# Optimization experiments

Measured on AMD Instinct MI355X. Metric: run time of the kernel, lower is better.

## Reference

```python
import jax, jax.numpy as jnp
import numpy as np

VOCAB = 128000
H = 256
L = 65536  # complete binary tree: 2**16 leaves -> 16 merge levels


def setup_inputs() -> dict:
    key = jax.random.key(0)
    ks = jax.random.split(key, 10)
    tokens = jax.random.randint(ks[0], (L,), 0, VOCAB)
    emb = jax.random.normal(ks[1], (VOCAB, H), dtype=jnp.float32) * 0.05
    # 5 gate projections per side (r_l, r_r, z_l, z_r, z), torch Linear layout (out, in)
    WL = jax.random.normal(ks[2], (5, H, H), dtype=jnp.float32) * 0.05
    WR = jax.random.normal(ks[3], (5, H, H), dtype=jnp.float32) * 0.05
    bL = jax.random.normal(ks[4], (5, H), dtype=jnp.float32) * 0.05
    bR = jax.random.normal(ks[5], (5, H), dtype=jnp.float32) * 0.05
    # candidate projections self.l / self.r
    Wlh = jax.random.normal(ks[6], (H, H), dtype=jnp.float32) * 0.05
    Wrh = jax.random.normal(ks[7], (H, H), dtype=jnp.float32) * 0.05
    blh = jax.random.normal(ks[8], (H,), dtype=jnp.float32) * 0.05
    brh = jax.random.normal(ks[9], (H,), dtype=jnp.float32) * 0.05
    return {"tokens": tokens, "emb": emb, "WL": WL, "WR": WR, "bL": bL,
            "bR": bR, "Wlh": Wlh, "Wrh": Wrh, "blh": blh, "brh": brh}


def reference(tokens, emb, WL, WR, bL, bR, Wlh, Wrh, blh, brh):
    cur = emb[tokens]  # [L, H] leaf states (embedding lookup)
    n_levels = int(np.log2(cur.shape[0]))
    bias = (bL + bR)[:, None, :]  # [5, 1, H]
    for _ in range(n_levels):
        left = cur[0::2]   # [N, H]
        right = cur[1::2]  # [N, H]
        # all 5 sigmoid gates in one batched contraction (torch Linear: x @ W.T + b)
        pre = (jnp.einsum('nh,goh->gno', left, WL)
               + jnp.einsum('nh,goh->gno', right, WR) + bias)  # [5, N, H]
        g = jax.nn.sigmoid(pre)
        r_l, r_r, z_l, z_r, z = g[0], g[1], g[2], g[3], g[4]
        h_tilde = jnp.tanh((r_l * left) @ Wlh.T + (r_r * right) @ Wrh.T + blh + brh)
        cur = z_l * left + z_r * right + z * h_tilde
    h = cur[0]  # [H] root state
    return (h, h, h)
```

## Files before the change

kernel.cpp:

```cpp
#include <hip/hip_runtime.h>
#include <hip/hip_bf16.h>

#define H 256
#define K2 512
#define BM 32
#define THREADS 512
#define HK2 (H * K2)

typedef __attribute__((ext_vector_type(8))) short short8;
typedef __attribute__((ext_vector_type(4))) float f32x4;

struct __align__(8) S4 { short x, y, z, w; };

__device__ __forceinline__ short f2bf(float f) {
    union { float f; unsigned u; } v; v.f = f;
    unsigned r = v.u + 0x7fffu + ((v.u >> 16) & 1u);
    return (short)(r >> 16);
}
__device__ __forceinline__ float bf2f(short s) {
    union { unsigned u; float f; } v; v.u = ((unsigned)(unsigned short)s) << 16;
    return v.f;
}
__device__ __forceinline__ float sigm(float x) {
    return 1.f / (1.f + __expf(-x));
}
__device__ __forceinline__ float tanh_f(float x) {
    float e = __expf(2.f * x);
    return 1.f - 2.f / (e + 1.f);
}
__device__ __forceinline__ int swz(int row, int kbytes) {
    return ((row << 10) + kbytes) ^ ((row & 7) << 4);
}

__global__ void prep_kernel(const float* __restrict__ WL, const float* __restrict__ WR,
                            const float* __restrict__ Wlh, const float* __restrict__ Wrh,
                            const float* __restrict__ bL, const float* __restrict__ bR,
                            const float* __restrict__ blh, const float* __restrict__ brh,
                            short* __restrict__ W1, short* __restrict__ W2,
                            float* __restrict__ pb, float* __restrict__ hb) {
    int i = blockIdx.x * blockDim.x + threadIdx.x;
    const int nW1 = 5 * HK2;
    if (i < nW1) {
        int g = i / HK2;
        int rem = i % HK2;
        int o = rem / K2, k = rem % K2;
        float v = (k < H) ? WL[(g * H + o) * H + k] : WR[(g * H + o) * H + (k - H)];
        W1[i] = f2bf(v);
        return;
    }
    int j = i - nW1;
    if (j < HK2) {
        int o = j / K2, k = j % K2;
        float v = (k < H) ? Wlh[o * H + k] : Wrh[o * H + (k - H)];
        W2[j] = f2bf(v);
        return;
    }
    int p = j - HK2;
    if (p < 5 * H) { pb[p] = bL[p] + bR[p]; return; }
    int q = p - 5 * H;
    if (q < H) { hb[q] = blh[q] + brh[q]; }
}

__global__ __launch_bounds__(THREADS, 2) void level_kernel(
    const float* __restrict__ curIn, const int* __restrict__ tokens,
    const float* __restrict__ emb, float* __restrict__ curOut,
    const short* __restrict__ W1, const short* __restrict__ W2,
    const float* __restrict__ pb, const float* __restrict__ hb, int N) {
    __shared__ __align__(16) short A1[BM * K2];
    __shared__ __align__(16) short A2[BM * K2];
    const int tid = threadIdx.x;
    const int n0 = blockIdx.x * BM;

#pragma unroll
    for (int it = 0; it < 8; ++it) {
        int c = tid + it * THREADS;
        int r = c >> 6;
        int col = (c & 63) << 2;
        int gr = 2 * n0 + r;
        float4 v = make_float4(0.f, 0.f, 0.f, 0.f);
        if (gr < 2 * N) {
            const float* src = tokens ? (emb + (size_t)tokens[gr] * H)
                                      : (curIn + (size_t)gr * H);
            v = *(const float4*)(src + col);
        }
        int row = r >> 1;
        int kel = ((r & 1) << 8) | col;
        S4 s; s.x = f2bf(v.x); s.y = f2bf(v.y); s.z = f2bf(v.z); s.w = f2bf(v.w);
        *(S4*)((char*)A1 + swz(row, kel * 2)) = s;
    }
    __syncthreads();

    const int wave = tid >> 6, lane = tid & 63;
    const int l15 = lane & 15, khalf = lane >> 4;
    const int col0 = wave * 32;

    f32x4 acc1[2][2][2];
#pragma unroll
    for (int g = 0; g < 2; ++g)
#pragma unroll
        for (int rt = 0; rt < 2; ++rt)
#pragma unroll
            for (int ct = 0; ct < 2; ++ct)
                acc1[g][rt][ct] = (f32x4){0.f, 0.f, 0.f, 0.f};

    const short* b1p[2][2];
#pragma unroll
    for (int g = 0; g < 2; ++g)
#pragma unroll
        for (int ct = 0; ct < 2; ++ct)
            b1p[g][ct] = W1 + g * HK2 + (size_t)(col0 + ct * 16 + l15) * K2 + khalf * 8;

#pragma unroll
    for (int kk = 0; kk < 16; ++kk) {
        short8 a[2];
#pragma unroll
        for (int rt = 0; rt < 2; ++rt)
            a[rt] = *(const short8*)((const char*)A1 + swz(rt * 16 + l15, kk * 64 + khalf * 16));
        short8 b[2][2];
#pragma unroll
        for (int g = 0; g < 2; ++g)
#pragma unroll
            for (int ct = 0; ct < 2; ++ct)
                b[g][ct] = *(const short8*)(b1p[g][ct] + kk * 32);
#pragma unroll
        for (int g = 0; g < 2; ++g)
#pragma unroll
            for (int rt = 0; rt < 2; ++rt)
#pragma unroll
                for (int ct = 0; ct < 2; ++ct)
                    acc1[g][rt][ct] = __builtin_amdgcn_mfma_f32_16x16x32_bf16(
                        a[rt], b[g][ct], acc1[g][rt][ct], 0, 0, 0);
    }

#pragma unroll
    for (int g = 0; g < 2; ++g)
#pragma unroll
        for (int ct = 0; ct < 2; ++ct) {
            int col = col0 + ct * 16 + l15;
            float bias = pb[g * H + col];
            int koff2 = ((g << 8) | col) * 2;
#pragma unroll
            for (int rt = 0; rt < 2; ++rt)
#pragma unroll
                for (int j = 0; j < 4; ++j) {
                    int row = rt * 16 + khalf * 4 + j;
                    float rg = sigm(acc1[g][rt][ct][j] + bias);
                    float xv = bf2f(*(const short*)((const char*)A1 + swz(row, koff2)));
                    *(short*)((char*)A2 + swz(row, koff2)) = f2bf(rg * xv);
                }
        }
    __syncthreads();

    f32x4 acc2[2][2];
#pragma unroll
    for (int rt = 0; rt < 2; ++rt)
#pragma unroll
        for (int ct = 0; ct < 2; ++ct)
            acc2[rt][ct] = (f32x4){0.f, 0.f, 0.f, 0.f};

    const short* b2p[2];
#pragma unroll
    for (int ct = 0; ct < 2; ++ct)
        b2p[ct] = W2 + (size_t)(col0 + ct * 16 + l15) * K2 + khalf * 8;

#pragma unroll
    for (int kk = 0; kk < 16; ++kk) {
        short8 a[2];
#pragma unroll
        for (int rt = 0; rt < 2; ++rt)
            a[rt] = *(const short8*)((const char*)A2 + swz(rt * 16 + l15, kk * 64 + khalf * 16));
        short8 b[2];
#pragma unroll
        for (int ct = 0; ct < 2; ++ct)
            b[ct] = *(const short8*)(b2p[ct] + kk * 32);
#pragma unroll
        for (int rt = 0; rt < 2; ++rt)
#pragma unroll
            for (int ct = 0; ct < 2; ++ct)
                acc2[rt][ct] = __builtin_amdgcn_mfma_f32_16x16x32_bf16(
                    a[rt], b[ct], acc2[rt][ct], 0, 0, 0);
    }

    float ht[2][2][4];
#pragma unroll
    for (int ct = 0; ct < 2; ++ct) {
        int col = col0 + ct * 16 + l15;
        float bias = hb[col];
#pragma unroll
        for (int rt = 0; rt < 2; ++rt)
#pragma unroll
            for (int j = 0; j < 4; ++j)
                ht[rt][ct][j] = tanh_f(acc2[rt][ct][j] + bias);
    }

    f32x4 acc3[3][2][2];
#pragma unroll
    for (int g = 0; g < 3; ++g)
#pragma unroll
        for (int rt = 0; rt < 2; ++rt)
#pragma unroll
            for (int ct = 0; ct < 2; ++ct)
                acc3[g][rt][ct] = (f32x4){0.f, 0.f, 0.f, 0.f};

    const short* b3p[3][2];
#pragma unroll
    for (int g = 0; g < 3; ++g)
#pragma unroll
        for (int ct = 0; ct < 2; ++ct)
            b3p[g][ct] = W1 + (g + 2) * HK2 + (size_t)(col0 + ct * 16 + l15) * K2 + khalf * 8;

#pragma unroll
    for (int kk = 0; kk < 16; ++kk) {
        short8 a[2];
#pragma unroll
        for (int rt = 0; rt < 2; ++rt)
            a[rt] = *(const short8*)((const char*)A1 + swz(rt * 16 + l15, kk * 64 + khalf * 16));
        short8 b[3][2];
#pragma unroll
        for (int g = 0; g < 3; ++g)
#pragma unroll
            for (int ct = 0; ct < 2; ++ct)
                b[g][ct] = *(const short8*)(b3p[g][ct] + kk * 32);
#pragma unroll
        for (int g = 0; g < 3; ++g)
#pragma unroll
            for (int rt = 0; rt < 2; ++rt)
#pragma unroll
                for (int ct = 0; ct < 2; ++ct)
                    acc3[g][rt][ct] = __builtin_amdgcn_mfma_f32_16x16x32_bf16(
                        a[rt], b[g][ct], acc3[g][rt][ct], 0, 0, 0);
    }

#pragma unroll
    for (int ct = 0; ct < 2; ++ct) {
        int col = col0 + ct * 16 + l15;
        float bzl = pb[2 * H + col];
        float bzr = pb[3 * H + col];
        float bzz = pb[4 * H + col];
#pragma unroll
        for (int rt = 0; rt < 2; ++rt)
#pragma unroll
            for (int j = 0; j < 4; ++j) {
                int row = rt * 16 + khalf * 4 + j;
                int gr = n0 + row;
                if (gr < N) {
                    float zl = sigm(acc3[0][rt][ct][j] + bzl);
                    float zr = sigm(acc3[1][rt][ct][j] + bzr);
                    float zz = sigm(acc3[2][rt][ct][j] + bzz);
                    float xl = bf2f(*(const short*)((const char*)A1 + swz(row, col * 2)));
                    float xr = bf2f(*(const short*)((const char*)A1 + swz(row, (col + 256) * 2)));
                    curOut[(size_t)gr * H + col] = zl * xl + zr * xr + zz * ht[rt][ct][j];
                }
            }
    }
}

__global__ void finalize_kernel(const float* __restrict__ h, float* __restrict__ out) {
    int i = threadIdx.x;
    if (i < 768) out[i] = h[i & 255];
}

extern "C" void kernel_launch(void* const* d_in, const int* in_sizes, int n_in,
                              void* d_out, int out_size, void* d_ws, size_t ws_size,
                              hipStream_t stream) {
    const int*   tokens = (const int*)d_in[0];
    const float* emb    = (const float*)d_in[1];
    const float* WL     = (const float*)d_in[2];
    const float* WR     = (const float*)d_in[3];
    const float* bL     = (const float*)d_in[4];
    const float* bR     = (const float*)d_in[5];
    const float* Wlh    = (const float*)d_in[6];
    const float* Wrh    = (const float*)d_in[7];
    const float* blh    = (const float*)d_in[8];
    const float* brh    = (const float*)d_in[9];

    char* ws = (char*)d_ws;
    short* W1 = (short*)ws;
    short* W2 = W1 + 5 * HK2;
    float* pb = (float*)(W2 + HK2);
    float* hb = pb + 5 * H;
    float* bufB = (float*)(ws + 2 * 1024 * 1024);
    float* bufA = bufB + (size_t)32768 * H;

    {
        int total = 5 * HK2 + HK2 + 5 * H + H;
        int blocks = (total + 255) / 256;
        prep_kernel<<<blocks, 256, 0, stream>>>(WL, WR, Wlh, Wrh, bL, bR, blh, brh,
                                                W1, W2, pb, hb);
    }

    const float* in = nullptr;
    for (int l = 0; l < 16; ++l) {
        int N = 32768 >> l;
        float* out = (l & 1) ? bufA : bufB;
        int blocks = (N + BM - 1) / BM;
        level_kernel<<<blocks, THREADS, 0, stream>>>(
            in, (l == 0) ? tokens : nullptr, emb, out, W1, W2, pb, hb, N);
        in = out;
    }

    finalize_kernel<<<1, 768, 0, stream>>>(bufA, (float*)d_out);
}
```

Before: 1.242 ms.

## Stream pre-tiled bf16 weights through triple-buffered LDS with async global-to-LDS loads

Weights are repacked into 96 contiguous 16KB tiles, ordered by MFMA fragment, and streamed into a three-slot LDS ring with global_load_lds. Each block issues these async loads while it runs MFMAs on the current tile. This replaces the per-lane direct global loads of B fragments. The six gate passes are fused into one loop: z_l, z_r and z first, then r_l and r_r, whose results overwrite A1 in place, then the candidate projection. This drops the A2 buffer and raises launch bounds to 4 blocks per CU. In exchange it adds two barriers per k-step and relies on hand-written waitcnt ordering. The prefetch also reads up to three tiles past the end, which is why the buffer is padded.

```diff
diff --git a/kernel.cpp b/kernel.cpp
--- a/kernel.cpp
+++ b/kernel.cpp
@@ -5,7 +5,9 @@
 #define K2 512
 #define BM 32
 #define THREADS 512
-#define HK2 (H * K2)
+#define TILE_B 16384
+#define NT 96
+#define NTP 99
 
 typedef __attribute__((ext_vector_type(8))) short short8;
 typedef __attribute__((ext_vector_type(4))) float f32x4;
@@ -21,53 +23,58 @@
     union { unsigned u; float f; } v; v.u = ((unsigned)(unsigned short)s) << 16;
     return v.f;
 }
-__device__ __forceinline__ float sigm(float x) {
-    return 1.f / (1.f + __expf(-x));
-}
+__device__ __forceinline__ float sigm(float x) { return 1.f / (1.f + __expf(-x)); }
 __device__ __forceinline__ float tanh_f(float x) {
     float e = __expf(2.f * x);
     return 1.f - 2.f / (e + 1.f);
 }
 __device__ __forceinline__ int swz(int row, int kbytes) {
     return ((row << 10) + kbytes) ^ ((row & 7) << 4);
+}
+__device__ __forceinline__ void gll16(const void* g, void* l) {
+    __builtin_amdgcn_global_load_lds((const __attribute__((address_space(1))) void*)g,
+                                     (__attribute__((address_space(3))) void*)l, 16, 0, 0);
 }
 
 __global__ void prep_kernel(const float* __restrict__ WL, const float* __restrict__ WR,
                             const float* __restrict__ Wlh, const float* __restrict__ Wrh,
                             const float* __restrict__ bL, const float* __restrict__ bR,
                             const float* __restrict__ blh, const float* __restrict__ brh,
-                            short* __restrict__ W1, short* __restrict__ W2,
-                            float* __restrict__ pb, float* __restrict__ hb) {
+                            short* __restrict__ Wp, float* __restrict__ pb,
+                            float* __restrict__ hb) {
     int i = blockIdx.x * blockDim.x + threadIdx.x;
-    const int nW1 = 5 * HK2;
-    if (i < nW1) {
-        int g = i / HK2;
-        int rem = i % HK2;
-        int o = rem / K2, k = rem % K2;
-        float v = (k < H) ? WL[(g * H + o) * H + k] : WR[(g * H + o) * H + (k - H)];
-        W1[i] = f2bf(v);
+    const int NW = NT * 8192;
+    if (i < NW) {
+        int T = i >> 13;
+        int r = i & 8191;
+        int khalf = r >> 11;
+        int col = (r >> 3) & 255;
+        int e = r & 7;
+        int p = T >> 4, kwin = T & 15;
+        int k = kwin * 32 + khalf * 8 + e;
+        float v;
+        if (p < 5) {
+            int g = (p < 3) ? (p + 2) : (p - 3);
+            v = (k < H) ? WL[(g * H + col) * H + k] : WR[(g * H + col) * H + (k - H)];
+        } else {
+            v = (k < H) ? Wlh[col * H + k] : Wrh[col * H + (k - H)];
+        }
+        Wp[i] = f2bf(v);
         return;
     }
-    int j = i - nW1;
-    if (j < HK2) {
-        int o = j / K2, k = j % K2;
-        float v = (k < H) ? Wlh[o * H + k] : Wrh[o * H + (k - H)];
-        W2[j] = f2bf(v);
-        return;
-    }
-    int p = j - HK2;
-    if (p < 5 * H) { pb[p] = bL[p] + bR[p]; return; }
-    int q = p - 5 * H;
+    int j = i - NW;
+    if (j < 5 * H) { pb[j] = bL[j] + bR[j]; return; }
+    int q = j - 5 * H;
     if (q < H) { hb[q] = blh[q] + brh[q]; }
 }
 
-__global__ __launch_bounds__(THREADS, 2) void level_kernel(
+__global__ __launch_bounds__(THREADS, 4) void level_kernel(
     const float* __restrict__ curIn, const int* __restrict__ tokens,
     const float* __restrict__ emb, float* __restrict__ curOut,
-    const short* __restrict__ W1, const short* __restrict__ W2,
-    const float* __restrict__ pb, const float* __restrict__ hb, int N) {
+    const short* __restrict__ Wp, const float* __restrict__ pb,
+    const float* __restrict__ hb, int N) {
     __shared__ __align__(16) short A1[BM * K2];
-    __shared__ __align__(16) short A2[BM * K2];
+    __shared__ __align__(16) short Bt[3 * 8192];
     const int tid = threadIdx.x;
     const int n0 = blockIdx.x * BM;
 
@@ -93,166 +100,147 @@
     const int wave = tid >> 6, lane = tid & 63;
     const int l15 = lane & 15, khalf = lane >> 4;
     const int col0 = wave * 32;
-
-    f32x4 acc1[2][2][2];
-#pragma unroll
-    for (int g = 0; g < 2; ++g)
+    const int bofs0 = khalf * 4096 + (col0 + l15) * 16;
+
+    {
+        const char* src = (const char*)Wp + tid * 16;
+        char* dst = (char*)Bt + tid * 16;
+        gll16(src, dst);                              gll16(src + 8192, dst + 8192);
+        gll16(src + TILE_B, dst + TILE_B);            gll16(src + TILE_B + 8192, dst + TILE_B + 8192);
+        gll16(src + 2 * TILE_B, dst + 2 * TILE_B);    gll16(src + 2 * TILE_B + 8192, dst + 2 * TILE_B + 8192);
+    }
+
+    float outv[2][2][4];
+    float zz[2][2][4];
+    f32x4 accRL[2][2];
+
+    for (int p = 0; p < 6; ++p) {
+        f32x4 acc[2][2];
 #pragma unroll
         for (int rt = 0; rt < 2; ++rt)
 #pragma unroll
             for (int ct = 0; ct < 2; ++ct)
-                acc1[g][rt][ct] = (f32x4){0.f, 0.f, 0.f, 0.f};
-
-    const short* b1p[2][2];
-#pragma unroll
-    for (int g = 0; g < 2; ++g)
-#pragma unroll
-        for (int ct = 0; ct < 2; ++ct)
-            b1p[g][ct] = W1 + g * HK2 + (size_t)(col0 + ct * 16 + l15) * K2 + khalf * 8;
-
-#pragma unroll
-    for (int kk = 0; kk < 16; ++kk) {
-        short8 a[2];
-#pragma unroll
-        for (int rt = 0; rt < 2; ++rt)
-            a[rt] = *(const short8*)((const char*)A1 + swz(rt * 16 + l15, kk * 64 + khalf * 16));
-        short8 b[2][2];
-#pragma unroll
-        for (int g = 0; g < 2; ++g)
-#pragma unroll
-            for (int ct = 0; ct < 2; ++ct)
-                b[g][ct] = *(const short8*)(b1p[g][ct] + kk * 32);
-#pragma unroll
-        for (int g = 0; g < 2; ++g)
+                acc[rt][ct] = (f32x4){0.f, 0.f, 0.f, 0.f};
+
+#pragma unroll
+        for (int kk = 0; kk < 16; ++kk) {
+            int t = p * 16 + kk;
+            int slot = t % 3;
+            asm volatile("s_waitcnt vmcnt(4)" ::: "memory");
+            __builtin_amdgcn_sched_barrier(0);
+            __builtin_amdgcn_s_barrier();
+            const char* Bb = (const char*)Bt + slot * TILE_B;
+            short8 a0 = *(const short8*)((const char*)A1 + swz(l15,      kk * 64 + khalf * 16));
+            short8 a1 = *(const short8*)((const char*)A1 + swz(16 + l15, kk * 64 + khalf * 16));
+            short8 b0 = *(const short8*)(Bb + bofs0);
+            short8 b1 = *(const short8*)(Bb + bofs0 + 256);
+            acc[0][0] = __builtin_amdgcn_mfma_f32_16x16x32_bf16(a0, b0, acc[0][0], 0, 0, 0);
+            acc[1][0] = __builtin_amdgcn_mfma_f32_16x16x32_bf16(a1, b0, acc[1][0], 0, 0, 0);
+            acc[0][1] = __builtin_amdgcn_mfma_f32_16x16x32_bf16(a0, b1, acc[0][1], 0, 0, 0);
+            acc[1][1] = __builtin_amdgcn_mfma_f32_16x16x32_bf16(a1, b1, acc[1][1], 0, 0, 0);
+            asm volatile("s_waitcnt lgkmcnt(0)" ::: "memory");
+            __builtin_amdgcn_sched_barrier(0);
+            __builtin_amdgcn_s_barrier();
+            __builtin_amdgcn_sched_barrier(0);
+            {
+                const char* src = (const char*)Wp + (size_t)(t + 3) * TILE_B + tid * 16;
+                char* dst = (char*)Bt + slot * TILE_B + tid * 16;
+                gll16(src, dst);
+                gll16(src + 8192, dst + 8192);
+            }
+        }
+
+        if (p == 0) {
+#pragma unroll
+            for (int ct = 0; ct < 2; ++ct) {
+                int col = col0 + ct * 16 + l15;
+                float bias = pb[2 * H + col];
+#pragma unroll
+                for (int rt = 0; rt < 2; ++rt)
+#pragma unroll
+                    for (int j = 0; j < 4; ++j) {
+                        int row = rt * 16 + khalf * 4 + j;
+                        float zl = sigm(acc[rt][ct][j] + bias);
+                        float xl = bf2f(*(const short*)((const char*)A1 + swz(row, col * 2)));
+                        outv[rt][ct][j] = zl * xl;
+                    }
+            }
+        } else if (p == 1) {
+#pragma unroll
+            for (int ct = 0; ct < 2; ++ct) {
+                int col = col0 + ct * 16 + l15;
+                float bias = pb[3 * H + col];
+#pragma unroll
+                for (int rt = 0; rt < 2; ++rt)
+#pragma unroll
+                    for (int j = 0; j < 4; ++j) {
+                        int row = rt * 16 + khalf * 4 + j;
+                        float zr = sigm(acc[rt][ct][j] + bias);
+                        float xr = bf2f(*(const short*)((const char*)A1 + swz(row, (col + 256) * 2)));
+                        outv[rt][ct][j] += zr * xr;
+                    }
+            }
+        } else if (p == 2) {
+#pragma unroll
+            for (int ct = 0; ct < 2; ++ct) {
+                int col = col0 + ct * 16 + l15;
+                float bias = pb[4 * H + col];
+#pragma unroll
+                for (int rt = 0; rt < 2; ++rt)
+#pragma unroll
+                    for (int j = 0; j < 4; ++j)
+                        zz[rt][ct][j] = sigm(acc[rt][ct][j] + bias);
+            }
+        } else if (p == 3) {
 #pragma unroll
             for (int rt = 0; rt < 2; ++rt)
 #pragma unroll
                 for (int ct = 0; ct < 2; ++ct)
-                    acc1[g][rt][ct] = __builtin_amdgcn_mfma_f32_16x16x32_bf16(
-                        a[rt], b[g][ct], acc1[g][rt][ct], 0, 0, 0);
-    }
-
-#pragma unroll
-    for (int g = 0; g < 2; ++g)
-#pragma unroll
-        for (int ct = 0; ct < 2; ++ct) {
-            int col = col0 + ct * 16 + l15;
-            float bias = pb[g * H + col];
-            int koff2 = ((g << 8) | col) * 2;
-#pragma unroll
-            for (int rt = 0; rt < 2; ++rt)
-#pragma unroll
-                for (int j = 0; j < 4; ++j) {
-                    int row = rt * 16 + khalf * 4 + j;
-                    float rg = sigm(acc1[g][rt][ct][j] + bias);
-                    float xv = bf2f(*(const short*)((const char*)A1 + swz(row, koff2)));
-                    *(short*)((char*)A2 + swz(row, koff2)) = f2bf(rg * xv);
-                }
-        }
-    __syncthreads();
-
-    f32x4 acc2[2][2];
-#pragma unroll
-    for (int rt = 0; rt < 2; ++rt)
-#pragma unroll
-        for (int ct = 0; ct < 2; ++ct)
-            acc2[rt][ct] = (f32x4){0.f, 0.f, 0.f, 0.f};
-
-    const short* b2p[2];
-#pragma unroll
-    for (int ct = 0; ct < 2; ++ct)
-        b2p[ct] = W2 + (size_t)(col0 + ct * 16 + l15) * K2 + khalf * 8;
-
-#pragma unroll
-    for (int kk = 0; kk < 16; ++kk) {
-        short8 a[2];
-#pragma unroll
-        for (int rt = 0; rt < 2; ++rt)
-            a[rt] = *(const short8*)((const char*)A2 + swz(rt * 16 + l15, kk * 64 + khalf * 16));
-        short8 b[2];
-#pragma unroll
-        for (int ct = 0; ct < 2; ++ct)
-            b[ct] = *(const short8*)(b2p[ct] + kk * 32);
-#pragma unroll
-        for (int rt = 0; rt < 2; ++rt)
-#pragma unroll
-            for (int ct = 0; ct < 2; ++ct)
-                acc2[rt][ct] = __builtin_amdgcn_mfma_f32_16x16x32_bf16(
-                    a[rt], b[ct], acc2[rt][ct], 0, 0, 0);
-    }
-
-    float ht[2][2][4];
-#pragma unroll
-    for (int ct = 0; ct < 2; ++ct) {
-        int col = col0 + ct * 16 + l15;
-        float bias = hb[col];
-#pragma unroll
-        for (int rt = 0; rt < 2; ++rt)
-#pragma unroll
-            for (int j = 0; j < 4; ++j)
-                ht[rt][ct][j] = tanh_f(acc2[rt][ct][j] + bias);
-    }
-
-    f32x4 acc3[3][2][2];
-#pragma unroll
-    for (int g = 0; g < 3; ++g)
-#pragma unroll
-        for (int rt = 0; rt < 2; ++rt)
-#pragma unroll
-            for (int ct = 0; ct < 2; ++ct)
-                acc3[g][rt][ct] = (f32x4){0.f, 0.f, 0.f, 0.f};
-
-    const short* b3p[3][2];
-#pragma unroll
-    for (int g = 0; g < 3; ++g)
-#pragma unroll
-        for (int ct = 0; ct < 2; ++ct)
-            b3p[g][ct] = W1 + (g + 2) * HK2 + (size_t)(col0 + ct * 16 + l15) * K2 + khalf * 8;
-
-#pragma unroll
-    for (int kk = 0; kk < 16; ++kk) {
-        short8 a[2];
-#pragma unroll
-        for (int rt = 0; rt < 2; ++rt)
-            a[rt] = *(const short8*)((const char*)A1 + swz(rt * 16 + l15, kk * 64 + khalf * 16));
-        short8 b[3][2];
-#pragma unroll
-        for (int g = 0; g < 3; ++g)
-#pragma unroll
-            for (int ct = 0; ct < 2; ++ct)
-                b[g][ct] = *(const short8*)(b3p[g][ct] + kk * 32);
-#pragma unroll
-        for (int g = 0; g < 3; ++g)
-#pragma unroll
-            for (int rt = 0; rt < 2; ++rt)
-#pragma unroll
-                for (int ct = 0; ct < 2; ++ct)
-                    acc3[g][rt][ct] = __builtin_amdgcn_mfma_f32_16x16x32_bf16(
-                        a[rt], b[g][ct], acc3[g][rt][ct], 0, 0, 0);
-    }
-
-#pragma unroll
-    for (int ct = 0; ct < 2; ++ct) {
-        int col = col0 + ct * 16 + l15;
-        float bzl = pb[2 * H + col];
-        float bzr = pb[3 * H + col];
-        float bzz = pb[4 * H + col];
-#pragma unroll
-        for (int rt = 0; rt < 2; ++rt)
-#pragma unroll
-            for (int j = 0; j < 4; ++j) {
-                int row = rt * 16 + khalf * 4 + j;
-                int gr = n0 + row;
-                if (gr < N) {
-                    float zl = sigm(acc3[0][rt][ct][j] + bzl);
-                    float zr = sigm(acc3[1][rt][ct][j] + bzr);
-                    float zz = sigm(acc3[2][rt][ct][j] + bzz);
-                    float xl = bf2f(*(const short*)((const char*)A1 + swz(row, col * 2)));
-                    float xr = bf2f(*(const short*)((const char*)A1 + swz(row, (col + 256) * 2)));
-                    curOut[(size_t)gr * H + col] = zl * xl + zr * xr + zz * ht[rt][ct][j];
-                }
-            }
-    }
+                    accRL[rt][ct] = acc[rt][ct];
+        } else if (p == 4) {
+#pragma unroll
+            for (int ct = 0; ct < 2; ++ct) {
+                int col = col0 + ct * 16 + l15;
+                float bl = pb[col];
+                float br = pb[H + col];
+#pragma unroll
+                for (int rt = 0; rt < 2; ++rt)
+#pragma unroll
+                    for (int j = 0; j < 4; ++j) {
+                        int row = rt * 16 + khalf * 4 + j;
+                        int aL = swz(row, col * 2);
+                        int aR = swz(row, (col + 256) * 2);
+                        float rl = sigm(accRL[rt][ct][j] + bl);
+                        float rr = sigm(acc[rt][ct][j] + br);
+                        float xl = bf2f(*(const short*)((const char*)A1 + aL));
+                        float xr = bf2f(*(const short*)((const char*)A1 + aR));
+                        *(short*)((char*)A1 + aL) = f2bf(rl * xl);
+                        *(short*)((char*)A1 + aR) = f2bf(rr * xr);
+                    }
+            }
+            asm volatile("s_waitcnt lgkmcnt(0)" ::: "memory");
+            __builtin_amdgcn_sched_barrier(0);
+            __builtin_amdgcn_s_barrier();
+        } else {
+#pragma unroll
+            for (int ct = 0; ct < 2; ++ct) {
+                int col = col0 + ct * 16 + l15;
+                float bias = hb[col];
+#pragma unroll
+                for (int rt = 0; rt < 2; ++rt)
+#pragma unroll
+                    for (int j = 0; j < 4; ++j) {
+                        int row = rt * 16 + khalf * 4 + j;
+                        int gr = n0 + row;
+                        float htv = tanh_f(acc[rt][ct][j] + bias);
+                        if (gr < N)
+                            curOut[(size_t)gr * H + col] =
+                                outv[rt][ct][j] + zz[rt][ct][j] * htv;
+                    }
+            }
+        }
+    }
+    asm volatile("s_waitcnt vmcnt(0) lgkmcnt(0)" ::: "memory");
 }
 
 __global__ void finalize_kernel(const float* __restrict__ h, float* __restrict__ out) {
@@ -275,18 +263,17 @@
     const float* brh    = (const float*)d_in[9];
 
     char* ws = (char*)d_ws;
-    short* W1 = (short*)ws;
-    short* W2 = W1 + 5 * HK2;
-    float* pb = (float*)(W2 + HK2);
+    short* Wp = (short*)ws;
+    float* pb = (float*)(ws + (size_t)NTP * TILE_B);
     float* hb = pb + 5 * H;
     float* bufB = (float*)(ws + 2 * 1024 * 1024);
     float* bufA = bufB + (size_t)32768 * H;
 
     {
-        int total = 5 * HK2 + HK2 + 5 * H + H;
+        int total = NT * 8192 + 5 * H + H;
         int blocks = (total + 255) / 256;
         prep_kernel<<<blocks, 256, 0, stream>>>(WL, WR, Wlh, Wrh, bL, bR, blh, brh,
-                                                W1, W2, pb, hb);
+                                                Wp, pb, hb);
     }
 
     const float* in = nullptr;
@@ -295,7 +282,7 @@
         float* out = (l & 1) ? bufA : bufB;
         int blocks = (N + BM - 1) / BM;
         level_kernel<<<blocks, THREADS, 0, stream>>>(
-            in, (l == 0) ? tokens : nullptr, emb, out, W1, W2, pb, hb, N);
+            in, (l == 0) ? tokens : nullptr, emb, out, Wp, pb, hb, N);
         in = out;
     }
 
```

Measured after the change: 1.399 ms. 12.6% more time.
